# Kernel tuning notes

Measured on AMD Instinct MI355X. Metric: run time of the kernel, lower is better.

The kernel has to match this reference:

```python
import jax, jax.numpy as jnp
import numpy as np

N_NODES = 50000
N_EDGES = 800000
IN_CH = 128
HID = 128


def setup_inputs() -> dict:
    key = jax.random.key(0)
    ks = jax.random.split(key, 16)
    inp = {
        "x": jax.random.normal(ks[0], (N_NODES, IN_CH), dtype=jnp.float32),
        "edge_index": jax.random.randint(ks[1], (2, N_EDGES), 0, N_NODES, dtype=jnp.int64),
        "batch_size": 1024,
    }
    dims = [(IN_CH, HID), (HID, HID), (HID, HID)]
    for i, (din, dout) in enumerate(dims):
        s = 1.0 / np.sqrt(din)
        inp[f"W_l{i}"] = jax.random.uniform(ks[2 + 4 * i], (dout, din), jnp.float32, -s, s)
        inp[f"b_l{i}"] = jax.random.uniform(ks[3 + 4 * i], (dout,), jnp.float32, -s, s)
        inp[f"W_r{i}"] = jax.random.uniform(ks[4 + 4 * i], (dout, din), jnp.float32, -s, s)
        inp[f"a{i}"] = jnp.full((dout,), 0.25, dtype=jnp.float32)  # PReLU slope
    return inp


def _sage_prelu(x, src, dst, W_l, b_l, W_r, a):
    # mean aggregation of source messages at target nodes
    msg_sum = jax.ops.segment_sum(x[src], dst, num_segments=N_NODES)  # [N, din]
    deg = jax.ops.segment_sum(jnp.ones((src.shape[0],), x.dtype), dst, num_segments=N_NODES)
    agg = msg_sum / jnp.maximum(deg, 1.0)[:, None]
    out = agg @ W_l.T + b_l + x @ W_r.T  # lin_l(aggr) + lin_r(x), bias on lin_l only
    return jnp.where(out > 0, out, a * out)  # per-channel PReLU


def reference(x, edge_index, batch_size, W_l0, b_l0, W_r0, a0, W_l1, b_l1, W_r1, a1, W_l2, b_l2, W_r2, a2):
    src, dst = edge_index[0], edge_index[1]
    x = _sage_prelu(x, src, dst, W_l0, b_l0, W_r0, a0)
    x = _sage_prelu(x, src, dst, W_l1, b_l1, W_r1, a1)
    x = _sage_prelu(x, src, dst, W_l2, b_l2, W_r2, a2)
    return x[:batch_size]
```

## Files before the change

kernel.cpp:

```cpp
#include <hip/hip_runtime.h>

#define NN 50000
#define NE 800000
#define C 128
#define CAP 64
#define EB2 ((NE / 2 + 255) / 256)
#define SPLITB 1563
#define WB 96
#define EB4 ((NE / 4 + 255) / 256)
#define ASTRIDE 136

typedef __attribute__((ext_vector_type(8))) short bf16x8;
typedef __attribute__((ext_vector_type(4))) float f32x4;
typedef unsigned short ushort;

__device__ inline ushort bf16_rn(float f) {
    unsigned u = __builtin_bit_cast(unsigned, f);
    u += 0x7FFF + ((u >> 16) & 1);
    return (ushort)(u >> 16);
}
__device__ inline void split_bf16(float f, ushort& hi, ushort& lo) {
    hi = bf16_rn(f);
    float hif = __builtin_bit_cast(float, (unsigned)hi << 16);
    lo = bf16_rn(f - hif);
}
__device__ inline float bf_lo(unsigned u) { return __builtin_bit_cast(float, u << 16); }
__device__ inline float bf_hi(unsigned u) { return __builtin_bit_cast(float, u & 0xFFFF0000u); }


__global__ __launch_bounds__(256)
void prep_kernel(const int* __restrict__ dst, const float* __restrict__ x,
                 const float* __restrict__ W0, const float* __restrict__ W1,
                 const float* __restrict__ W2, const float* __restrict__ W3,
                 const float* __restrict__ W4, const float* __restrict__ W5,
                 int* __restrict__ deg, int* __restrict__ pos,
                 ushort* __restrict__ Ah, ushort* __restrict__ Al,
                 ushort* __restrict__ Wh, ushort* __restrict__ Wl) {
    int t = threadIdx.x;
    if (blockIdx.x < EB2) {
        int e0 = (blockIdx.x * 256 + t) * 2;
        if (e0 < NE) {
            int2 d2 = *(const int2*)(dst + e0);
            int p0 = atomicAdd(&deg[d2.x], 1);
            int p1 = atomicAdd(&deg[d2.y], 1);
            *(int2*)(pos + e0) = make_int2(p0, p1);
        }
    } else if (blockIdx.x < EB2 + SPLITB) {
        int tid = (blockIdx.x - EB2) * 256 + t;
        const int total = NN * C / 4;
        for (int i = tid; i < total; i += SPLITB * 256) {
            f32x4 v = ((const f32x4*)x)[i];
            ushort h0, h1, h2, h3, l0, l1, l2, l3;
            split_bf16(v.x, h0, l0);
            split_bf16(v.y, h1, l1);
            split_bf16(v.z, h2, l2);
            split_bf16(v.w, h3, l3);
            *(uint2*)(Ah + (size_t)i * 4) = make_uint2((unsigned)h0 | ((unsigned)h1 << 16),
                                                       (unsigned)h2 | ((unsigned)h3 << 16));
            *(uint2*)(Al + (size_t)i * 4) = make_uint2((unsigned)l0 | ((unsigned)l1 << 16),
                                                       (unsigned)l2 | ((unsigned)l3 << 16));
        }
    } else {
        const float* Ws[6] = {W0, W1, W2, W3, W4, W5};
        int i = (blockIdx.x - EB2 - SPLITB) * 256 + t;
        int mat = i >> 12;
        f32x4 v = ((const f32x4*)Ws[mat])[i & 4095];
        ushort h0, h1, h2, h3, l0, l1, l2, l3;
        split_bf16(v.x, h0, l0);
        split_bf16(v.y, h1, l1);
        split_bf16(v.z, h2, l2);
        split_bf16(v.w, h3, l3);
        *(uint2*)(Wh + (size_t)i * 4) = make_uint2((unsigned)h0 | ((unsigned)h1 << 16),
                                                   (unsigned)h2 | ((unsigned)h3 << 16));
        *(uint2*)(Wl + (size_t)i * 4) = make_uint2((unsigned)l0 | ((unsigned)l1 << 16),
                                                   (unsigned)l2 | ((unsigned)l3 << 16));
    }
}


__global__ __launch_bounds__(256)
void fill_kernel(const int* __restrict__ src, const int* __restrict__ dst,
                 const int* __restrict__ pos, int* __restrict__ col) {
    int e0 = (blockIdx.x * 256 + threadIdx.x) * 4;
    if (e0 >= NE) return;
    int4 da = *(const int4*)(dst + e0);
    int4 sa = *(const int4*)(src + e0);
    int4 pa = *(const int4*)(pos + e0);
    if (pa.x < CAP) col[da.x * CAP + pa.x] = sa.x;
    if (pa.y < CAP) col[da.y * CAP + pa.y] = sa.y;
    if (pa.z < CAP) col[da.z * CAP + pa.z] = sa.z;
    if (pa.w < CAP) col[da.w * CAP + pa.w] = sa.w;
}


__global__ __launch_bounds__(256)
void agg_kernel(const ushort* __restrict__ xh, const int* __restrict__ deg,
                const int* __restrict__ col,
                ushort* __restrict__ aggh, ushort* __restrict__ aggl, int nodes) {
    int node = (blockIdx.x * blockDim.x + threadIdx.x) >> 6;
    int lane = threadIdx.x & 63;
    if (node >= nodes) return;
    int quad = lane >> 4;
    int ql   = lane & 15;
    int d = min(deg[node], CAP);
    int start = node * CAP;
    int end = start + d;
    const uint4* xr = (const uint4*)xh;
    float a0=0,a1=0,a2=0,a3=0,a4=0,a5=0,a6=0,a7=0;
    int e = start;
    for (; e + 7 < end; e += 8) {
        int i0 = col[e + quad];
        int i1 = col[e + 4 + quad];
        uint4 u0 = xr[(size_t)i0 * 16 + ql];
        uint4 u1 = xr[(size_t)i1 * 16 + ql];
        a0 += bf_lo(u0.x) + bf_lo(u1.x); a1 += bf_hi(u0.x) + bf_hi(u1.x);
        a2 += bf_lo(u0.y) + bf_lo(u1.y); a3 += bf_hi(u0.y) + bf_hi(u1.y);
        a4 += bf_lo(u0.z) + bf_lo(u1.z); a5 += bf_hi(u0.z) + bf_hi(u1.z);
        a6 += bf_lo(u0.w) + bf_lo(u1.w); a7 += bf_hi(u0.w) + bf_hi(u1.w);
    }
    for (; e + 3 < end; e += 4) {
        uint4 u = xr[(size_t)col[e + quad] * 16 + ql];
        a0 += bf_lo(u.x); a1 += bf_hi(u.x);
        a2 += bf_lo(u.y); a3 += bf_hi(u.y);
        a4 += bf_lo(u.z); a5 += bf_hi(u.z);
        a6 += bf_lo(u.w); a7 += bf_hi(u.w);
    }
    int rem = end - e;
    if (quad < rem) {
        uint4 u = xr[(size_t)col[e + quad] * 16 + ql];
        a0 += bf_lo(u.x); a1 += bf_hi(u.x);
        a2 += bf_lo(u.y); a3 += bf_hi(u.y);
        a4 += bf_lo(u.z); a5 += bf_hi(u.z);
        a6 += bf_lo(u.w); a7 += bf_hi(u.w);
    }
    a0 += __shfl_xor(a0, 16, 64); a0 += __shfl_xor(a0, 32, 64);
    a1 += __shfl_xor(a1, 16, 64); a1 += __shfl_xor(a1, 32, 64);
    a2 += __shfl_xor(a2, 16, 64); a2 += __shfl_xor(a2, 32, 64);
    a3 += __shfl_xor(a3, 16, 64); a3 += __shfl_xor(a3, 32, 64);
    a4 += __shfl_xor(a4, 16, 64); a4 += __shfl_xor(a4, 32, 64);
    a5 += __shfl_xor(a5, 16, 64); a5 += __shfl_xor(a5, 32, 64);
    a6 += __shfl_xor(a6, 16, 64); a6 += __shfl_xor(a6, 32, 64);
    a7 += __shfl_xor(a7, 16, 64); a7 += __shfl_xor(a7, 32, 64);
    if (quad == 0) {
        float inv = 1.0f / (float)max(d, 1);
        float m[8] = {a0*inv, a1*inv, a2*inv, a3*inv, a4*inv, a5*inv, a6*inv, a7*inv};
        ushort h[8], o[8];
        #pragma unroll
        for (int j = 0; j < 8; ++j) split_bf16(m[j], h[j], o[j]);
        size_t off = (size_t)node * C + ql * 8;
        *(uint4*)(aggh + off) = make_uint4((unsigned)h[0] | ((unsigned)h[1] << 16),
                                           (unsigned)h[2] | ((unsigned)h[3] << 16),
                                           (unsigned)h[4] | ((unsigned)h[5] << 16),
                                           (unsigned)h[6] | ((unsigned)h[7] << 16));
        *(uint4*)(aggl + off) = make_uint4((unsigned)o[0] | ((unsigned)o[1] << 16),
                                           (unsigned)o[2] | ((unsigned)o[3] << 16),
                                           (unsigned)o[4] | ((unsigned)o[5] << 16),
                                           (unsigned)o[6] | ((unsigned)o[7] << 16));
    }
}


__global__ __launch_bounds__(256, 3)
void gemm_kernel(const ushort* __restrict__ Ah, const ushort* __restrict__ Al,
                 const ushort* __restrict__ Xh, const ushort* __restrict__ Xl,
                 const ushort* __restrict__ Wlh, const ushort* __restrict__ Wll,
                 const ushort* __restrict__ Wrh, const ushort* __restrict__ Wrl,
                 const float* __restrict__ bl, const float* __restrict__ slope,
                 float* __restrict__ outf, ushort* __restrict__ outh,
                 ushort* __restrict__ outl, int rows) {
    __shared__ ushort Ahi[64 * ASTRIDE];
    __shared__ ushort Alo[64 * ASTRIDE];
    int t = threadIdx.x;
    int lane = t & 63;
    int w = t >> 6;
    int l = lane & 15;
    int q = lane >> 4;
    int row0 = blockIdx.x * 64;

    f32x4 acc[4][2];
    #pragma unroll
    for (int mt = 0; mt < 4; ++mt)
        #pragma unroll
        for (int nt = 0; nt < 2; ++nt)
            acc[mt][nt] = (f32x4){0.f, 0.f, 0.f, 0.f};

    #pragma unroll
    for (int mat = 0; mat < 2; ++mat) {
        const ushort* WH = mat ? Wrh : Wlh;
        const ushort* WL = mat ? Wrl : Wll;
        const ushort* Ph = mat ? Xh : Ah;
        const ushort* Pl = mat ? Xl : Al;

        bf16x8 bhi[2][4], blo[2][4];
        #pragma unroll
        for (int nt = 0; nt < 2; ++nt) {
            int n = w * 32 + nt * 16 + l;
            const ushort* wp = WH + (size_t)n * C + q * 8;
            const ushort* wq = WL + (size_t)n * C + q * 8;
            #pragma unroll
            for (int kb = 0; kb < 4; ++kb) {
                bhi[nt][kb] = *(const bf16x8*)(wp + kb * 32);
                blo[nt][kb] = *(const bf16x8*)(wq + kb * 32);
            }
        }

        __syncthreads();
        int ar = t >> 2;
        int aq = t & 3;
        int r = min(row0 + ar, rows - 1);
        ushort* dh = Ahi + ar * ASTRIDE + aq * 32;
        ushort* dl = Alo + ar * ASTRIDE + aq * 32;
        const ushort* ph = Ph + (size_t)r * C + aq * 32;
        const ushort* pl = Pl + (size_t)r * C + aq * 32;
        #pragma unroll
        for (int i = 0; i < 4; ++i) {
            *(uint4*)(dh + i * 8) = *(const uint4*)(ph + i * 8);
            *(uint4*)(dl + i * 8) = *(const uint4*)(pl + i * 8);
        }
        __syncthreads();

        #pragma unroll
        for (int kb = 0; kb < 4; ++kb) {
            #pragma unroll
            for (int mt = 0; mt < 4; ++mt) {
                int off = (mt * 16 + l) * ASTRIDE + kb * 32 + q * 8;
                bf16x8 ahi = *(const bf16x8*)(Ahi + off);
                bf16x8 alo = *(const bf16x8*)(Alo + off);
                #pragma unroll
                for (int nt = 0; nt < 2; ++nt) {
                    acc[mt][nt] = __builtin_amdgcn_mfma_f32_16x16x32_bf16(ahi, bhi[nt][kb], acc[mt][nt], 0, 0, 0);
                    acc[mt][nt] = __builtin_amdgcn_mfma_f32_16x16x32_bf16(alo, bhi[nt][kb], acc[mt][nt], 0, 0, 0);
                    acc[mt][nt] = __builtin_amdgcn_mfma_f32_16x16x32_bf16(ahi, blo[nt][kb], acc[mt][nt], 0, 0, 0);
                }
            }
        }
    }

    #pragma unroll
    for (int nt = 0; nt < 2; ++nt) {
        int n = w * 32 + nt * 16 + l;
        float b = bl[n], s = slope[n];
        #pragma unroll
        for (int mt = 0; mt < 4; ++mt) {
            #pragma unroll
            for (int rg = 0; rg < 4; ++rg) {
                int r = row0 + mt * 16 + q * 4 + rg;
                if (r < rows) {
                    float v = acc[mt][nt][rg] + b;
                    v = v > 0.f ? v : s * v;
                    if (outf) {
                        outf[(size_t)r * C + n] = v;
                    } else {
                        ushort hh, ll;
                        split_bf16(v, hh, ll);
                        outh[(size_t)r * C + n] = hh;
                        outl[(size_t)r * C + n] = ll;
                    }
                }
            }
        }
    }
}


extern "C" void kernel_launch(void* const* d_in, const int* in_sizes, int n_in,
                              void* d_out, int out_size, void* d_ws, size_t ws_size,
                              hipStream_t stream) {
    const float* x   = (const float*)d_in[0];
    const int*   src = (const int*)d_in[1];
    const int*   dst = src + NE;
    const float* Wl[3] = {(const float*)d_in[3], (const float*)d_in[7],  (const float*)d_in[11]};
    const float* bl[3] = {(const float*)d_in[4], (const float*)d_in[8],  (const float*)d_in[12]};
    const float* Wr[3] = {(const float*)d_in[5], (const float*)d_in[9],  (const float*)d_in[13]};
    const float* sl[3] = {(const float*)d_in[6], (const float*)d_in[10], (const float*)d_in[14]};

    int*   deg     = (int*)d_ws;
    int*   pos     = deg + 50016;
    int*   col     = pos + 800000;
    ushort* Whs    = (ushort*)(col + NN * CAP);
    ushort* Wls    = Whs + 6 * 16384;
    ushort* Gh     = Wls + 6 * 16384;
    ushort* Gl     = Gh + (size_t)NN * C;
    ushort* Ah     = Gl + (size_t)NN * C;
    ushort* Al     = Ah + (size_t)NN * C;
    ushort* Bh     = Al + (size_t)NN * C;
    ushort* Bl     = Bh + (size_t)NN * C;

    hipMemsetAsync(deg, 0, 50016 * sizeof(int), stream);

    prep_kernel<<<EB2 + SPLITB + WB, 256, 0, stream>>>(
        dst, x, Wl[0], Wr[0], Wl[1], Wr[1], Wl[2], Wr[2],
        deg, pos, Ah, Al, Whs, Wls);
    fill_kernel<<<EB4, 256, 0, stream>>>(src, dst, pos, col);

    int rows_out = out_size / C;

    agg_kernel<<<(NN + 3) / 4, 256, 0, stream>>>(Ah, deg, col, Gh, Gl, NN);
    gemm_kernel<<<(NN + 63) / 64, 256, 0, stream>>>(Gh, Gl, Ah, Al,
                                                    Whs + 0 * 16384, Wls + 0 * 16384,
                                                    Whs + 1 * 16384, Wls + 1 * 16384,
                                                    bl[0], sl[0], nullptr, Bh, Bl, NN);

    agg_kernel<<<(NN + 3) / 4, 256, 0, stream>>>(Bh, deg, col, Gh, Gl, NN);
    gemm_kernel<<<(NN + 63) / 64, 256, 0, stream>>>(Gh, Gl, Bh, Bl,
                                                    Whs + 2 * 16384, Wls + 2 * 16384,
                                                    Whs + 3 * 16384, Wls + 3 * 16384,
                                                    bl[1], sl[1], nullptr, Ah, Al, NN);

    agg_kernel<<<(rows_out + 3) / 4, 256, 0, stream>>>(Ah, deg, col, Gh, Gl, rows_out);
    gemm_kernel<<<(rows_out + 63) / 64, 256, 0, stream>>>(Gh, Gl, Ah, Al,
                                                          Whs + 4 * 16384, Wls + 4 * 16384,
                                                          Whs + 5 * 16384, Wls + 5 * 16384,
                                                          bl[2], sl[2], (float*)d_out, nullptr, nullptr,
                                                          rows_out);
}
```

Baseline: 296.1 us.

## Restrict layer-two aggregation and GEMM to the output nodes' receptive field

Adds a mark kernel that flags the first rows_out nodes and their in-neighbors, and a compact kernel that turns those flags into a node list. The layer-two aggregation and GEMM take this list and process only the flagged nodes, gathering and scattering rows through it. The goal is to avoid computing layer-two features that the final output never reads. The cost is two extra small launches, a larger memset, atomic-based list building in nondeterministic order, and indirect row access in the GEMM.

```diff
diff --git a/kernel.cpp b/kernel.cpp
--- a/kernel.cpp
+++ b/kernel.cpp
@@ -94,12 +94,38 @@
 
 
 __global__ __launch_bounds__(256)
+void mark_kernel(const int* __restrict__ deg, const int* __restrict__ col,
+                 int* __restrict__ needed, int rows_out) {
+    int i = blockIdx.x * 256 + threadIdx.x;
+    int n = i / CAP;
+    int s = i - n * CAP;
+    if (n >= rows_out) return;
+    if (s == 0) needed[n] = 1;
+    if (s < min(deg[n], CAP)) needed[col[n * CAP + s]] = 1;
+}
+
+
+__global__ __launch_bounds__(256)
+void compact_kernel(const int* __restrict__ needed, int* __restrict__ list,
+                    int* __restrict__ cnt) {
+    int i = blockIdx.x * 256 + threadIdx.x;
+    if (i < NN && needed[i]) {
+        int p = atomicAdd(cnt, 1);
+        list[p] = i;
+    }
+}
+
+
+__global__ __launch_bounds__(256)
 void agg_kernel(const ushort* __restrict__ xh, const int* __restrict__ deg,
                 const int* __restrict__ col,
+                const int* __restrict__ list, const int* __restrict__ countp,
                 ushort* __restrict__ aggh, ushort* __restrict__ aggl, int nodes) {
-    int node = (blockIdx.x * blockDim.x + threadIdx.x) >> 6;
+    int i = (blockIdx.x * blockDim.x + threadIdx.x) >> 6;
     int lane = threadIdx.x & 63;
-    if (node >= nodes) return;
+    int cnt = list ? *countp : nodes;
+    if (i >= cnt) return;
+    int node = list ? list[i] : i;
     int quad = lane >> 4;
     int ql   = lane & 15;
     int d = min(deg[node], CAP);
@@ -166,6 +192,7 @@
                  const ushort* __restrict__ Wlh, const ushort* __restrict__ Wll,
                  const ushort* __restrict__ Wrh, const ushort* __restrict__ Wrl,
                  const float* __restrict__ bl, const float* __restrict__ slope,
+                 const int* __restrict__ list, const int* __restrict__ countp,
                  float* __restrict__ outf, ushort* __restrict__ outh,
                  ushort* __restrict__ outl, int rows) {
     __shared__ ushort Ahi[64 * ASTRIDE];
@@ -176,6 +203,8 @@
     int l = lane & 15;
     int q = lane >> 4;
     int row0 = blockIdx.x * 64;
+    int cnt = list ? min(*countp, rows) : rows;
+    if (row0 >= cnt) return;
 
     f32x4 acc[4][2];
     #pragma unroll
@@ -207,7 +236,8 @@
         __syncthreads();
         int ar = t >> 2;
         int aq = t & 3;
-        int r = min(row0 + ar, rows - 1);
+        int ridx = min(row0 + ar, cnt - 1);
+        int r = list ? list[ridx] : ridx;
         ushort* dh = Ahi + ar * ASTRIDE + aq * 32;
         ushort* dl = Alo + ar * ASTRIDE + aq * 32;
         const ushort* ph = Ph + (size_t)r * C + aq * 32;
@@ -244,8 +274,9 @@
         for (int mt = 0; mt < 4; ++mt) {
             #pragma unroll
             for (int rg = 0; rg < 4; ++rg) {
-                int r = row0 + mt * 16 + q * 4 + rg;
-                if (r < rows) {
+                int ridx = row0 + mt * 16 + q * 4 + rg;
+                if (ridx < cnt) {
+                    int r = list ? list[ridx] : ridx;
                     float v = acc[mt][nt][rg] + b;
                     v = v > 0.f ? v : s * v;
                     if (outf) {
@@ -275,9 +306,12 @@
     const float* sl[3] = {(const float*)d_in[6], (const float*)d_in[10], (const float*)d_in[14]};
 
     int*   deg     = (int*)d_ws;
-    int*   pos     = deg + 50016;
+    int*   needed  = deg + 50016;
+    int*   cnt     = needed + 50016;
+    int*   pos     = cnt + 16;
     int*   col     = pos + 800000;
-    ushort* Whs    = (ushort*)(col + NN * CAP);
+    int*   list    = col + NN * CAP;
+    ushort* Whs    = (ushort*)(list + 50016);
     ushort* Wls    = Whs + 6 * 16384;
     ushort* Gh     = Wls + 6 * 16384;
     ushort* Gl     = Gh + (size_t)NN * C;
@@ -286,31 +320,38 @@
     ushort* Bh     = Al + (size_t)NN * C;
     ushort* Bl     = Bh + (size_t)NN * C;
 
-    hipMemsetAsync(deg, 0, 50016 * sizeof(int), stream);
+    int rows_out = out_size / C;
+
+    hipMemsetAsync(deg, 0, (2 * 50016 + 16) * sizeof(int), stream);
 
     prep_kernel<<<EB2 + SPLITB + WB, 256, 0, stream>>>(
         dst, x, Wl[0], Wr[0], Wl[1], Wr[1], Wl[2], Wr[2],
         deg, pos, Ah, Al, Whs, Wls);
     fill_kernel<<<EB4, 256, 0, stream>>>(src, dst, pos, col);
 
-    int rows_out = out_size / C;
-
-    agg_kernel<<<(NN + 3) / 4, 256, 0, stream>>>(Ah, deg, col, Gh, Gl, NN);
+    mark_kernel<<<(rows_out * CAP + 255) / 256, 256, 0, stream>>>(deg, col, needed, rows_out);
+    compact_kernel<<<(NN + 255) / 256, 256, 0, stream>>>(needed, list, cnt);
+
+    agg_kernel<<<(NN + 3) / 4, 256, 0, stream>>>(Ah, deg, col, nullptr, nullptr, Gh, Gl, NN);
     gemm_kernel<<<(NN + 63) / 64, 256, 0, stream>>>(Gh, Gl, Ah, Al,
                                                     Whs + 0 * 16384, Wls + 0 * 16384,
                                                     Whs + 1 * 16384, Wls + 1 * 16384,
-                                                    bl[0], sl[0], nullptr, Bh, Bl, NN);
-
-    agg_kernel<<<(NN + 3) / 4, 256, 0, stream>>>(Bh, deg, col, Gh, Gl, NN);
+                                                    bl[0], sl[0], nullptr, nullptr,
+                                                    nullptr, Bh, Bl, NN);
+
+    agg_kernel<<<(NN + 3) / 4, 256, 0, stream>>>(Bh, deg, col, list, cnt, Gh, Gl, NN);
     gemm_kernel<<<(NN + 63) / 64, 256, 0, stream>>>(Gh, Gl, Bh, Bl,
                                                     Whs + 2 * 16384, Wls + 2 * 16384,
                                                     Whs + 3 * 16384, Wls + 3 * 16384,
-                                                    bl[1], sl[1], nullptr, Ah, Al, NN);
-
-    agg_kernel<<<(rows_out + 3) / 4, 256, 0, stream>>>(Ah, deg, col, Gh, Gl, rows_out);
+                                                    bl[1], sl[1], list, cnt,
+                                                    nullptr, Ah, Al, NN);
+
+    agg_kernel<<<(rows_out + 3) / 4, 256, 0, stream>>>(Ah, deg, col, nullptr, nullptr,
+                                                       Gh, Gl, rows_out);
     gemm_kernel<<<(rows_out + 63) / 64, 256, 0, stream>>>(Gh, Gl, Ah, Al,
                                                           Whs + 4 * 16384, Wls + 4 * 16384,
                                                           Whs + 5 * 16384, Wls + 5 * 16384,
-                                                          bl[2], sl[2], (float*)d_out, nullptr, nullptr,
+                                                          bl[2], sl[2], nullptr, nullptr,
+                                                          (float*)d_out, nullptr, nullptr,
                                                           rows_out);
 }
```

After: 292.9 us. Within noise of the previous version (-1.1%).
